# Performance work log

Measured on AMD Instinct MI355X. Metric: run time of the kernel, lower is better.

The kernel has to match this reference:

```python
import jax, jax.numpy as jnp
import numpy as np

CLIP = 100000.0
T, N, C, H, E = 8, 1024, 64, 256, 32768
NC = N * (N + 1) // 2


def _ntn(t):
    return jnp.nan_to_num(t, nan=0.0, posinf=CLIP, neginf=-CLIP)


def _gcn_conv(x, row, col, ew, W, b, n):
    # PyG GCNConv: sym-normalized aggregation (self-loops already appended)
    h = x @ W  # [n, out]
    deg = jax.ops.segment_sum(ew, col, num_segments=n)
    dinv = jnp.where(deg > 0, jax.lax.rsqrt(jnp.where(deg > 0, deg, 1.0)), 0.0)
    norm = dinv[row] * ew * dinv[col]  # [e]
    out = jax.ops.segment_sum(norm[:, None] * h[row], col, num_segments=n)
    return out + b


def setup_inputs() -> dict:
    key = jax.random.key(0)
    ks = jax.random.split(key, 10)
    return {
        "xs": jax.random.normal(ks[0], (T, N, C), jnp.float32),
        "edge_index": jax.random.randint(ks[1], (T, 2, E), 0, N),
        "edge_weight": jax.random.uniform(ks[2], (T, E), jnp.float32),
        "conv1_w": jax.random.normal(ks[3], (C, H), jnp.float32) * 0.05,
        "conv1_b": jnp.zeros((H,), jnp.float32),
        "conv2_w": jax.random.normal(ks[4], (H, H), jnp.float32) * 0.05,
        "conv2_b": jnp.zeros((H,), jnp.float32),
        "w_ih": jax.random.normal(ks[5], (4 * H, H), jnp.float32) * 0.05,
        "w_hh": jax.random.normal(ks[6], (4 * H, H), jnp.float32) * 0.05,
        "b_ih": jnp.zeros((4 * H,), jnp.float32),
        "b_hh": jnp.zeros((4 * H,), jnp.float32),
        "fc_w": jax.random.normal(ks[7], (H, NC), jnp.float32) * 0.02,
        "fc_b": jnp.zeros((NC,), jnp.float32),
    }


def reference(xs, edge_index, edge_weight, conv1_w, conv1_b, conv2_w, conv2_b,
              w_ih, w_hh, b_ih, b_hh, fc_w, fc_b):
    n = xs.shape[1]
    self_idx = jnp.arange(n)

    def per_step(x, ei, ew):
        # add self-loops with weight 1 (GCNConv default)
        row = jnp.concatenate([ei[0], self_idx])
        col = jnp.concatenate([ei[1], self_idx])
        w = jnp.concatenate([ew, jnp.ones((n,), ew.dtype)])
        h = jax.nn.relu(_ntn(_gcn_conv(x, row, col, w, conv1_w, conv1_b, n)))
        h = jax.nn.relu(_ntn(_gcn_conv(h, row, col, w, conv2_w, conv2_b, n)))
        return _ntn(h.mean(axis=0))  # global mean pool, single graph

    embs = _ntn(jax.vmap(per_step)(xs, edge_index, edge_weight))  # [T, H]

    def lstm_step(carry, x_t):
        h, c = carry
        g = x_t @ w_ih.T + b_ih + h @ w_hh.T + b_hh
        i, f, gg, o = jnp.split(g, 4)
        c = jax.nn.sigmoid(f) * c + jax.nn.sigmoid(i) * jnp.tanh(gg)
        h = jax.nn.sigmoid(o) * jnp.tanh(c)
        return (h, c), h

    hdim = w_hh.shape[1]
    init = (jnp.zeros((hdim,), embs.dtype), jnp.zeros((hdim,), embs.dtype))
    _, hs = jax.lax.scan(lstm_step, init, embs)
    final_h = _ntn(_ntn(hs)[-1])  # [H]

    vec = _ntn(final_h @ fc_w + fc_b)  # [N(N+1)/2]
    tril = jnp.tril_indices(n)  # row-major (i, j<=i) matches torch loop
    L = jnp.zeros((n, n), vec.dtype).at[tril].set(vec)
    return _ntn(L @ L.T)
```

## Files before the change

### kernel.cpp

```cpp
#include <hip/hip_runtime.h>
#include <hip/hip_bf16.h>
#include <math.h>

#define T_ 8
#define N_ 1024
#define C_ 64
#define H_ 256
#define E_ 32768
#define NC_ 524800
#define CLIPV 100000.0f

__device__ __forceinline__ float sigmoidf_(float x) { return 1.0f / (1.0f + __expf(-x)); }

__global__ void init_kernel(float* deg, int* cnt, float* cbuf, float* pool_part) {
    int g = blockIdx.x * 256 + threadIdx.x;
    if (g < T_ * N_) { deg[g] = 1.0f; cnt[g] = 0; }
    if (g < 512) cbuf[g] = 0.0f;
    if (g < T_ * 32 * H_) pool_part[g] = 0.0f;
}

__global__ void deg_count_kernel(const int* ei, const float* ew, float* deg, int* cnt) {
    int g = blockIdx.x * 256 + threadIdx.x;
    int t = g >> 15, e = g & (E_ - 1);
    int col = ei[t * 2 * E_ + E_ + e];
    atomicAdd(&deg[t * N_ + col], ew[g]);
    atomicAdd(&cnt[t * N_ + col], 1);
}

__global__ void dinv_kernel(float* deg) {
    int g = blockIdx.x * 256 + threadIdx.x;
    deg[g] = rsqrtf(deg[g]);
}

__global__ __launch_bounds__(1024) void scan_kernel(const int* cnt, int* ptr, int* cursor) {
    __shared__ int s[1024];
    int t = blockIdx.x, tid = threadIdx.x;
    int c0 = cnt[t * N_ + tid];
    s[tid] = c0;
    __syncthreads();
    for (int off = 1; off < 1024; off <<= 1) {
        int v = (tid >= off) ? s[tid - off] : 0;
        __syncthreads();
        s[tid] += v;
        __syncthreads();
    }
    int excl = s[tid] - c0;
    ptr[t * N_ + tid] = excl;
    cursor[t * N_ + tid] = excl;
}

__global__ void scatter_kernel(const int* ei, const float* ew, const float* dinv,
                               int* cursor, int* csr_src, float* csr_nrm) {
    int g = blockIdx.x * 256 + threadIdx.x;
    int t = g >> 15, e = g & (E_ - 1);
    int row = ei[t * 2 * E_ + e];
    int col = ei[t * 2 * E_ + E_ + e];
    int pos = atomicAdd(&cursor[t * N_ + col], 1);
    csr_src[t * E_ + pos] = row;
    csr_nrm[t * E_ + pos] = ew[g] * dinv[t * N_ + row];
}

__global__ __launch_bounds__(256) void sgemm_nn(const float* __restrict__ A,
                                                const float* __restrict__ B,
                                                float* __restrict__ C,
                                                int M, int N, int K) {
    __shared__ float As[16][68];
    __shared__ float Bs[16][68];
    int tid = threadIdx.x;
    int tx = tid & 15, ty = tid >> 4;
    int m0 = blockIdx.y * 64, n0 = blockIdx.x * 64;
    float acc[4][4] = {{0.f}};
    for (int k0 = 0; k0 < K; k0 += 16) {
        int ka = tid & 15, ma = tid >> 4;
#pragma unroll
        for (int mm = 0; mm < 64; mm += 16)
            As[ka][ma + mm] = A[(size_t)(m0 + ma + mm) * K + k0 + ka];
        int nb = tid & 63, kb = tid >> 6;
#pragma unroll
        for (int kk = 0; kk < 16; kk += 4)
            Bs[kb + kk][nb] = B[(size_t)(k0 + kb + kk) * N + n0 + nb];
        __syncthreads();
#pragma unroll
        for (int kk = 0; kk < 16; ++kk) {
            float4 a4 = *(const float4*)&As[kk][ty * 4];
            float4 b4 = *(const float4*)&Bs[kk][tx * 4];
            float a[4] = {a4.x, a4.y, a4.z, a4.w};
            float b[4] = {b4.x, b4.y, b4.z, b4.w};
#pragma unroll
            for (int i = 0; i < 4; ++i)
#pragma unroll
                for (int j = 0; j < 4; ++j) acc[i][j] += a[i] * b[j];
        }
        __syncthreads();
    }
#pragma unroll
    for (int i = 0; i < 4; ++i) {
        float4 o = make_float4(acc[i][0], acc[i][1], acc[i][2], acc[i][3]);
        *(float4*)&C[(size_t)(m0 + ty * 4 + i) * N + n0 + tx * 4] = o;
    }
}

template <bool POOL>
__global__ __launch_bounds__(256) void agg_kernel(const float* __restrict__ hin,
                                                  const float* __restrict__ dinv,
                                                  const int* __restrict__ ptr,
                                                  const int* __restrict__ cnt,
                                                  const int* __restrict__ csr_src,
                                                  const float* __restrict__ csr_nrm,
                                                  const float* __restrict__ bias,
                                                  float* __restrict__ out) {
    __shared__ int s_src[256];
    __shared__ float s_nrm[256];
    int bx = blockIdx.x;
    int t = bx >> 10, j = bx & 1023;
    int c = threadIdx.x;
    float dj = dinv[bx];
    int start = ptr[bx], count = cnt[bx];
    const float* hbase = hin + (size_t)(t * N_) * H_;
    float self = hin[(size_t)bx * H_ + c];
    float accE = 0.0f;
    for (int base = 0; base < count; base += 256) {
        int m = min(256, count - base);
        __syncthreads();
        if (c < m) {
            s_src[c] = csr_src[t * E_ + start + base + c];
            s_nrm[c] = csr_nrm[t * E_ + start + base + c];
        }
        __syncthreads();
        for (int u = 0; u < m; ++u)
            accE += s_nrm[u] * hbase[(size_t)s_src[u] * H_ + c];
    }
    float val = dj * (dj * self + accE) + bias[c];
    val = fminf(fmaxf(val, 0.0f), CLIPV);
    if (POOL)
        atomicAdd(&out[(size_t)(t * 32 + (j & 31)) * H_ + c], val * (1.0f / 1024.0f));
    else
        out[(size_t)bx * H_ + c] = val;
}

__global__ void pool_final_kernel(const float* pool_part, float* embs) {
    int t = blockIdx.x, c = threadIdx.x;
    float a = 0.f;
#pragma unroll
    for (int g2 = 0; g2 < 32; ++g2) a += pool_part[(size_t)(t * 32 + g2) * H_ + c];
    a = fminf(fmaxf(a, -CLIPV), CLIPV);
    embs[t * H_ + c] = a;
}

__global__ __launch_bounds__(256) void xg_kernel(const float* __restrict__ embs,
                                                 const float* __restrict__ w_ih,
                                                 const float* __restrict__ b_ih,
                                                 const float* __restrict__ b_hh,
                                                 float* __restrict__ xg) {
    __shared__ float s_e[H_];
    int b = blockIdx.x;
    int t = b >> 2;
    int j = (b & 3) * 256 + threadIdx.x;
    s_e[threadIdx.x] = embs[t * H_ + threadIdx.x];
    __syncthreads();
    const float4* wr = (const float4*)(w_ih + (size_t)j * H_);
    float acc = b_ih[j] + b_hh[j];
#pragma unroll 4
    for (int k4 = 0; k4 < H_ / 4; ++k4) {
        float4 w = wr[k4];
        acc += w.x * s_e[k4 * 4] + w.y * s_e[k4 * 4 + 1] + w.z * s_e[k4 * 4 + 2] + w.w * s_e[k4 * 4 + 3];
    }
    xg[t * 1024 + j] = acc;
}

__global__ __launch_bounds__(256) void lstm_step_kernel(const float* __restrict__ xg,
                                                        const float* __restrict__ w_hh,
                                                        float* __restrict__ gates,
                                                        float* __restrict__ cbuf,
                                                        float* __restrict__ final_h,
                                                        int step) {
    __shared__ float s_h[H_];
    int tid = threadIdx.x;
    if (step == 0) {
        s_h[tid] = 0.0f;
    } else {
        const float* gp = gates + ((step - 1) & 1) * 1024;
        float gi = gp[tid], gf = gp[256 + tid], gg = gp[512 + tid], go = gp[768 + tid];
        float cprev = cbuf[(step & 1) * 256 + tid];
        float cc = sigmoidf_(gf) * cprev + sigmoidf_(gi) * tanhf(gg);
        float hh = sigmoidf_(go) * tanhf(cc);
        if (blockIdx.x == 0) cbuf[((step + 1) & 1) * 256 + tid] = cc;
        if (step == T_) {
            if (blockIdx.x == 0) final_h[tid] = hh;
            return;
        }
        s_h[tid] = hh;
    }
    __syncthreads();
    int j = blockIdx.x * 256 + tid;
    const float4* wr = (const float4*)(w_hh + (size_t)j * H_);
    float acc = xg[step * 1024 + j];
#pragma unroll 4
    for (int k4 = 0; k4 < H_ / 4; ++k4) {
        float4 w = wr[k4];
        acc += w.x * s_h[k4 * 4] + w.y * s_h[k4 * 4 + 1] + w.z * s_h[k4 * 4 + 2] + w.w * s_h[k4 * 4 + 3];
    }
    gates[(step & 1) * 1024 + j] = acc;
}

__global__ __launch_bounds__(256) void fc_kernel(const float* __restrict__ final_h,
                                                 const float* __restrict__ fc_w,
                                                 const float* __restrict__ fc_b,
                                                 float* __restrict__ vec) {
    __shared__ float s_h[H_];
    s_h[threadIdx.x] = final_h[threadIdx.x];
    __syncthreads();
    int j4 = blockIdx.x * 256 + threadIdx.x;
    if (j4 >= NC_ / 4) return;
    const float4* w4 = (const float4*)fc_w;
    float4 acc = ((const float4*)fc_b)[j4];
#pragma unroll 4
    for (int k = 0; k < H_; ++k) {
        float4 w = w4[(size_t)k * (NC_ / 4) + j4];
        float hk = s_h[k];
        acc.x += hk * w.x; acc.y += hk * w.y; acc.z += hk * w.z; acc.w += hk * w.w;
    }
    acc.x = fminf(fmaxf(acc.x, -CLIPV), CLIPV);
    acc.y = fminf(fmaxf(acc.y, -CLIPV), CLIPV);
    acc.z = fminf(fmaxf(acc.z, -CLIPV), CLIPV);
    acc.w = fminf(fmaxf(acc.w, -CLIPV), CLIPV);
    ((float4*)vec)[j4] = acc;
}

__global__ void build_L_kernel(const float* __restrict__ vec, float* __restrict__ L) {
    int g = blockIdx.x * 256 + threadIdx.x;
    int i = g >> 10, j = g & 1023;
    float v = 0.0f;
    if (j <= i) v = vec[(i * (i + 1)) / 2 + j];
    L[g] = v;
}

__global__ __launch_bounds__(256) void syrk_kernel(const float* __restrict__ L, float* __restrict__ Cout) {
    int b = blockIdx.x;
    int I = (int)((sqrtf(8.0f * b + 1.0f) - 1.0f) * 0.5f);
    while ((I + 1) * (I + 2) / 2 <= b) ++I;
    while (I * (I + 1) / 2 > b) --I;
    int J = b - I * (I + 1) / 2;
    int Klim = (J + 1) * 64;
    int kbeg = blockIdx.y * 256;
    int kend = min(Klim, kbeg + 256);
    if (kbeg >= kend) return;

    __shared__ float As[16][68];
    __shared__ float Bs[16][68];
    int tid = threadIdx.x;
    int tx = tid & 15, ty = tid >> 4;
    int m0 = I * 64, n0 = J * 64;
    float acc[4][4] = {{0.f}};
    for (int k0 = kbeg; k0 < kend; k0 += 16) {
        int ka = tid & 15, ma = tid >> 4;
#pragma unroll
        for (int mm = 0; mm < 64; mm += 16) {
            As[ka][ma + mm] = L[(size_t)(m0 + ma + mm) * 1024 + k0 + ka];
            Bs[ka][ma + mm] = L[(size_t)(n0 + ma + mm) * 1024 + k0 + ka];
        }
        __syncthreads();
#pragma unroll
        for (int kk = 0; kk < 16; ++kk) {
            float4 a4 = *(const float4*)&As[kk][ty * 4];
            float4 b4 = *(const float4*)&Bs[kk][tx * 4];
            float a[4] = {a4.x, a4.y, a4.z, a4.w};
            float bb[4] = {b4.x, b4.y, b4.z, b4.w};
#pragma unroll
            for (int i = 0; i < 4; ++i)
#pragma unroll
                for (int j = 0; j < 4; ++j) acc[i][j] += a[i] * bb[j];
        }
        __syncthreads();
    }
#pragma unroll
    for (int i = 0; i < 4; ++i)
#pragma unroll
        for (int j = 0; j < 4; ++j)
            atomicAdd(&Cout[(size_t)(m0 + ty * 4 + i) * 1024 + n0 + tx * 4 + j], acc[i][j]);
}

__global__ __launch_bounds__(256) void mirror_kernel(float* __restrict__ Cout) {
    int J = blockIdx.x, I = blockIdx.y;
    if (J >= I) return;
    __shared__ float s[64][65];
    int cc = threadIdx.x & 63, r0 = threadIdx.x >> 6;
    for (int r = r0; r < 64; r += 4)
        s[r][cc] = Cout[(size_t)(I * 64 + r) * 1024 + J * 64 + cc];
    __syncthreads();
    for (int r = r0; r < 64; r += 4)
        Cout[(size_t)(J * 64 + r) * 1024 + I * 64 + cc] = s[cc][r];
}

extern "C" void kernel_launch(void* const* d_in, const int* in_sizes, int n_in,
                              void* d_out, int out_size, void* d_ws, size_t ws_size,
                              hipStream_t stream) {
    const float* xs      = (const float*)d_in[0];
    const int*   ei      = (const int*)d_in[1];
    const float* ew      = (const float*)d_in[2];
    const float* conv1_w = (const float*)d_in[3];
    const float* conv1_b = (const float*)d_in[4];
    const float* conv2_w = (const float*)d_in[5];
    const float* conv2_b = (const float*)d_in[6];
    const float* w_ih    = (const float*)d_in[7];
    const float* w_hh    = (const float*)d_in[8];
    const float* b_ih    = (const float*)d_in[9];
    const float* b_hh    = (const float*)d_in[10];
    const float* fc_w    = (const float*)d_in[11];
    const float* fc_b    = (const float*)d_in[12];
    float* out = (float*)d_out;

    float* ws = (float*)d_ws;
    size_t off = 0;
    float* xw1  = ws + off; off += (size_t)T_ * N_ * H_;
    float* h1   = ws + off; off += (size_t)T_ * N_ * H_;
    float* vec  = h1;
    float* Lm   = h1 + NC_;
    float* deg  = ws + off; off += T_ * N_;
    float* csr_nrm = ws + off; off += (size_t)T_ * E_;
    float* pool_part = ws + off; off += T_ * 32 * H_;
    float* embs = ws + off; off += T_ * H_;
    float* xg   = ws + off; off += T_ * 4 * H_;
    float* gates = ws + off; off += 2 * 1024;
    float* cbuf  = ws + off; off += 2 * 256;
    float* final_h = ws + off; off += 256;
    int* cnt    = (int*)(ws + off); off += T_ * N_;
    int* ptr    = (int*)(ws + off); off += T_ * N_;
    int* cursor = (int*)(ws + off); off += T_ * N_;
    int* csr_src = (int*)(ws + off); off += (size_t)T_ * E_;
    (void)ws_size; (void)in_sizes; (void)n_in; (void)out_size;

    init_kernel<<<256, 256, 0, stream>>>(deg, cnt, cbuf, pool_part);
    deg_count_kernel<<<(T_ * E_) / 256, 256, 0, stream>>>(ei, ew, deg, cnt);
    dinv_kernel<<<(T_ * N_) / 256, 256, 0, stream>>>(deg);
    scan_kernel<<<T_, 1024, 0, stream>>>(cnt, ptr, cursor);
    scatter_kernel<<<(T_ * E_) / 256, 256, 0, stream>>>(ei, ew, deg, cursor, csr_src, csr_nrm);

    sgemm_nn<<<dim3(H_ / 64, (T_ * N_) / 64), 256, 0, stream>>>(xs, conv1_w, xw1, T_ * N_, H_, C_);
    agg_kernel<false><<<T_ * N_, 256, 0, stream>>>(xw1, deg, ptr, cnt, csr_src, csr_nrm, conv1_b, h1);
    sgemm_nn<<<dim3(H_ / 64, (T_ * N_) / 64), 256, 0, stream>>>(h1, conv2_w, xw1, T_ * N_, H_, H_);
    agg_kernel<true><<<T_ * N_, 256, 0, stream>>>(xw1, deg, ptr, cnt, csr_src, csr_nrm, conv2_b, pool_part);
    pool_final_kernel<<<T_, 256, 0, stream>>>(pool_part, embs);

    xg_kernel<<<32, 256, 0, stream>>>(embs, w_ih, b_ih, b_hh, xg);
    for (int s = 0; s < T_; ++s)
        lstm_step_kernel<<<4, 256, 0, stream>>>(xg, w_hh, gates, cbuf, final_h, s);
    lstm_step_kernel<<<1, 256, 0, stream>>>(xg, w_hh, gates, cbuf, final_h, T_);

    fc_kernel<<<(NC_ / 4 + 255) / 256, 256, 0, stream>>>(final_h, fc_w, fc_b, vec);
    build_L_kernel<<<(N_ * N_) / 256, 256, 0, stream>>>(vec, Lm);

    hipMemsetAsync(d_out, 0, (size_t)N_ * N_ * sizeof(float), stream);
    syrk_kernel<<<dim3(136, 4), 256, 0, stream>>>(Lm, out);
    mirror_kernel<<<dim3(16, 16), 256, 0, stream>>>(out);
}
```

Measured before the change: 346.5 us.

## Fuse small kernels, persist LSTM with grid barrier, scatter FC directly into L

Several small kernels are merged to cut launch overhead: init becomes a memset, dinv folds into a warp-shuffle scan, pool reduction folds into the xg kernel, and the eight LSTM step launches become one persistent kernel. That kernel keeps w_hh in registers and synchronises its four blocks with a spin-wait global barrier. The FC kernel computes two quads per thread and writes directly into the lower-triangular L matrix, removing the separate build_L pass. The aggregation loop is unrolled by four with independent accumulators, which changes the summation order. The spin barrier assumes all four blocks are co-resident and has a timeout escape.

```diff
diff --git a/kernel.cpp b/kernel.cpp
--- a/kernel.cpp
+++ b/kernel.cpp
@@ -12,13 +12,6 @@
 
 __device__ __forceinline__ float sigmoidf_(float x) { return 1.0f / (1.0f + __expf(-x)); }
 
-__global__ void init_kernel(float* deg, int* cnt, float* cbuf, float* pool_part) {
-    int g = blockIdx.x * 256 + threadIdx.x;
-    if (g < T_ * N_) { deg[g] = 1.0f; cnt[g] = 0; }
-    if (g < 512) cbuf[g] = 0.0f;
-    if (g < T_ * 32 * H_) pool_part[g] = 0.0f;
-}
-
 __global__ void deg_count_kernel(const int* ei, const float* ew, float* deg, int* cnt) {
     int g = blockIdx.x * 256 + threadIdx.x;
     int t = g >> 15, e = g & (E_ - 1);
@@ -27,26 +20,35 @@
     atomicAdd(&cnt[t * N_ + col], 1);
 }
 
-__global__ void dinv_kernel(float* deg) {
-    int g = blockIdx.x * 256 + threadIdx.x;
-    deg[g] = rsqrtf(deg[g]);
-}
-
-__global__ __launch_bounds__(1024) void scan_kernel(const int* cnt, int* ptr, int* cursor) {
-    __shared__ int s[1024];
+__global__ __launch_bounds__(1024) void scan_dinv_kernel(const int* cnt, int* ptr, int* cursor,
+                                                         float* deg) {
+    __shared__ int s_wsum[16];
     int t = blockIdx.x, tid = threadIdx.x;
+    int lane = tid & 63, w = tid >> 6;
     int c0 = cnt[t * N_ + tid];
-    s[tid] = c0;
-    __syncthreads();
-    for (int off = 1; off < 1024; off <<= 1) {
-        int v = (tid >= off) ? s[tid - off] : 0;
-        __syncthreads();
-        s[tid] += v;
-        __syncthreads();
-    }
-    int excl = s[tid] - c0;
+    int x = c0;
+#pragma unroll
+    for (int off = 1; off < 64; off <<= 1) {
+        int v = __shfl_up(x, off);
+        if (lane >= off) x += v;
+    }
+    if (lane == 63) s_wsum[w] = x;
+    __syncthreads();
+    if (tid < 16) {
+        int v = s_wsum[tid];
+#pragma unroll
+        for (int off = 1; off < 16; off <<= 1) {
+            int u = __shfl_up(v, off);
+            if (tid >= off) v += u;
+        }
+        s_wsum[tid] = v;
+    }
+    __syncthreads();
+    int base = (w > 0) ? s_wsum[w - 1] : 0;
+    int excl = base + x - c0;
     ptr[t * N_ + tid] = excl;
     cursor[t * N_ + tid] = excl;
+    deg[t * N_ + tid] = rsqrtf(deg[t * N_ + tid] + 1.0f);
 }
 
 __global__ void scatter_kernel(const int* ei, const float* ew, const float* dinv,
@@ -118,7 +120,7 @@
     int start = ptr[bx], count = cnt[bx];
     const float* hbase = hin + (size_t)(t * N_) * H_;
     float self = hin[(size_t)bx * H_ + c];
-    float accE = 0.0f;
+    float a0 = 0.f, a1 = 0.f, a2 = 0.f, a3 = 0.f;
     for (int base = 0; base < count; base += 256) {
         int m = min(256, count - base);
         __syncthreads();
@@ -127,9 +129,18 @@
             s_nrm[c] = csr_nrm[t * E_ + start + base + c];
         }
         __syncthreads();
-        for (int u = 0; u < m; ++u)
-            accE += s_nrm[u] * hbase[(size_t)s_src[u] * H_ + c];
-    }
+        int u = 0;
+        for (; u + 3 < m; u += 4) {
+            int s0 = s_src[u], s1 = s_src[u + 1], s2 = s_src[u + 2], s3 = s_src[u + 3];
+            float n0 = s_nrm[u], n1 = s_nrm[u + 1], n2 = s_nrm[u + 2], n3 = s_nrm[u + 3];
+            a0 += n0 * hbase[(size_t)s0 * H_ + c];
+            a1 += n1 * hbase[(size_t)s1 * H_ + c];
+            a2 += n2 * hbase[(size_t)s2 * H_ + c];
+            a3 += n3 * hbase[(size_t)s3 * H_ + c];
+        }
+        for (; u < m; ++u) a0 += s_nrm[u] * hbase[(size_t)s_src[u] * H_ + c];
+    }
+    float accE = (a0 + a1) + (a2 + a3);
     float val = dj * (dj * self + accE) + bias[c];
     val = fminf(fmaxf(val, 0.0f), CLIPV);
     if (POOL)
@@ -138,25 +149,20 @@
         out[(size_t)bx * H_ + c] = val;
 }
 
-__global__ void pool_final_kernel(const float* pool_part, float* embs) {
-    int t = blockIdx.x, c = threadIdx.x;
-    float a = 0.f;
-#pragma unroll
-    for (int g2 = 0; g2 < 32; ++g2) a += pool_part[(size_t)(t * 32 + g2) * H_ + c];
-    a = fminf(fmaxf(a, -CLIPV), CLIPV);
-    embs[t * H_ + c] = a;
-}
-
-__global__ __launch_bounds__(256) void xg_kernel(const float* __restrict__ embs,
-                                                 const float* __restrict__ w_ih,
-                                                 const float* __restrict__ b_ih,
-                                                 const float* __restrict__ b_hh,
-                                                 float* __restrict__ xg) {
+__global__ __launch_bounds__(256) void xg_pool_kernel(const float* __restrict__ pool_part,
+                                                      const float* __restrict__ w_ih,
+                                                      const float* __restrict__ b_ih,
+                                                      const float* __restrict__ b_hh,
+                                                      float* __restrict__ xg) {
     __shared__ float s_e[H_];
     int b = blockIdx.x;
     int t = b >> 2;
-    int j = (b & 3) * 256 + threadIdx.x;
-    s_e[threadIdx.x] = embs[t * H_ + threadIdx.x];
+    int tid = threadIdx.x;
+    int j = (b & 3) * 256 + tid;
+    float a = 0.f;
+#pragma unroll
+    for (int g2 = 0; g2 < 32; ++g2) a += pool_part[(size_t)(t * 32 + g2) * H_ + tid];
+    s_e[tid] = fminf(fmaxf(a, -CLIPV), CLIPV);
     __syncthreads();
     const float4* wr = (const float4*)(w_ih + (size_t)j * H_);
     float acc = b_ih[j] + b_hh[j];
@@ -168,71 +174,120 @@
     xg[t * 1024 + j] = acc;
 }
 
-__global__ __launch_bounds__(256) void lstm_step_kernel(const float* __restrict__ xg,
+__device__ __forceinline__ void gbar(int* bar, int target) {
+    __syncthreads();
+    if (threadIdx.x == 0) {
+        __threadfence();
+        __hip_atomic_fetch_add(bar, 1, __ATOMIC_ACQ_REL, __HIP_MEMORY_SCOPE_AGENT);
+        long spin = 0;
+        while (__hip_atomic_load(bar, __ATOMIC_ACQUIRE, __HIP_MEMORY_SCOPE_AGENT) < target) {
+            if (++spin > (1L << 27)) break;
+        }
+    }
+    __syncthreads();
+}
+
+__global__ __launch_bounds__(1024) void lstm_all_kernel(const float* __restrict__ xg,
                                                         const float* __restrict__ w_hh,
-                                                        float* __restrict__ gates,
-                                                        float* __restrict__ cbuf,
-                                                        float* __restrict__ final_h,
-                                                        int step) {
+                                                        float* __restrict__ gbuf,
+                                                        int* __restrict__ bar,
+                                                        float* __restrict__ final_h) {
     __shared__ float s_h[H_];
     int tid = threadIdx.x;
-    if (step == 0) {
-        s_h[tid] = 0.0f;
+    int jl = tid >> 2, q = tid & 3;
+    int j = blockIdx.x * 256 + jl;
+    float4 wreg[16];
+    const float4* wr = (const float4*)(w_hh + (size_t)j * H_ + q * 64);
+#pragma unroll
+    for (int r = 0; r < 16; ++r) wreg[r] = wr[r];
+    float c_reg = 0.f;
+    for (int s = 0; s < T_; ++s) {
+        if (s == 0) {
+            if (tid < 256) s_h[tid] = 0.f;
+        } else {
+            if (tid < 256) {
+                const float* gp = gbuf + ((s - 1) & 1) * 1024;
+                float gi = gp[tid], gf = gp[256 + tid], gg = gp[512 + tid], go = gp[768 + tid];
+                c_reg = sigmoidf_(gf) * c_reg + sigmoidf_(gi) * tanhf(gg);
+                s_h[tid] = sigmoidf_(go) * tanhf(c_reg);
+            }
+        }
+        __syncthreads();
+        float acc = 0.f;
+#pragma unroll
+        for (int r = 0; r < 16; ++r) {
+            float4 w = wreg[r];
+            int k = q * 64 + r * 4;
+            acc += w.x * s_h[k] + w.y * s_h[k + 1] + w.z * s_h[k + 2] + w.w * s_h[k + 3];
+        }
+        acc += __shfl_xor(acc, 1);
+        acc += __shfl_xor(acc, 2);
+        if (q == 0) gbuf[(s & 1) * 1024 + j] = xg[s * 1024 + j] + acc;
+        gbar(bar, 4 * (s + 1));
+    }
+    if (blockIdx.x == 0 && tid < 256) {
+        const float* gp = gbuf + ((T_ - 1) & 1) * 1024;
+        float gi = gp[tid], gf = gp[256 + tid], gg = gp[512 + tid], go = gp[768 + tid];
+        float cc = sigmoidf_(gf) * c_reg + sigmoidf_(gi) * tanhf(gg);
+        final_h[tid] = sigmoidf_(go) * tanhf(cc);
+    }
+}
+
+__device__ __forceinline__ void store_quad(float4 v, int j0, float* __restrict__ Lm) {
+    int i = (int)((sqrtf(8.0f * (float)j0 + 1.0f) - 1.0f) * 0.5f);
+    while ((i + 1) * (i + 2) / 2 <= j0) ++i;
+    while (i * (i + 1) / 2 > j0) --i;
+    int rb = i * (i + 1) / 2, col = j0 - rb;
+    if (col + 3 <= i) {
+        *(float4*)&Lm[(size_t)i * 1024 + col] = v;
     } else {
-        const float* gp = gates + ((step - 1) & 1) * 1024;
-        float gi = gp[tid], gf = gp[256 + tid], gg = gp[512 + tid], go = gp[768 + tid];
-        float cprev = cbuf[(step & 1) * 256 + tid];
-        float cc = sigmoidf_(gf) * cprev + sigmoidf_(gi) * tanhf(gg);
-        float hh = sigmoidf_(go) * tanhf(cc);
-        if (blockIdx.x == 0) cbuf[((step + 1) & 1) * 256 + tid] = cc;
-        if (step == T_) {
-            if (blockIdx.x == 0) final_h[tid] = hh;
-            return;
-        }
-        s_h[tid] = hh;
-    }
-    __syncthreads();
-    int j = blockIdx.x * 256 + tid;
-    const float4* wr = (const float4*)(w_hh + (size_t)j * H_);
-    float acc = xg[step * 1024 + j];
-#pragma unroll 4
-    for (int k4 = 0; k4 < H_ / 4; ++k4) {
-        float4 w = wr[k4];
-        acc += w.x * s_h[k4 * 4] + w.y * s_h[k4 * 4 + 1] + w.z * s_h[k4 * 4 + 2] + w.w * s_h[k4 * 4 + 3];
-    }
-    gates[(step & 1) * 1024 + j] = acc;
+        float vv[4] = {v.x, v.y, v.z, v.w};
+#pragma unroll
+        for (int e = 0; e < 4; ++e) {
+            int jj = j0 + e;
+            while ((i + 1) * (i + 2) / 2 <= jj) ++i;
+            Lm[(size_t)i * 1024 + (jj - i * (i + 1) / 2)] = vv[e];
+        }
+    }
 }
 
 __global__ __launch_bounds__(256) void fc_kernel(const float* __restrict__ final_h,
                                                  const float* __restrict__ fc_w,
                                                  const float* __restrict__ fc_b,
-                                                 float* __restrict__ vec) {
+                                                 float* __restrict__ Lm) {
     __shared__ float s_h[H_];
-    s_h[threadIdx.x] = final_h[threadIdx.x];
-    __syncthreads();
-    int j4 = blockIdx.x * 256 + threadIdx.x;
-    if (j4 >= NC_ / 4) return;
+    int tid = threadIdx.x;
+    s_h[tid] = final_h[tid];
+    __syncthreads();
+    const int NQ = NC_ / 4;
+    int j4a = blockIdx.x * 512 + tid;
+    int j4b = j4a + 256;
+    bool va = j4a < NQ, vb = j4b < NQ;
+    int j4b_eff = vb ? j4b : j4a;
+    if (!va) return;
     const float4* w4 = (const float4*)fc_w;
-    float4 acc = ((const float4*)fc_b)[j4];
+    float4 accA = ((const float4*)fc_b)[j4a];
+    float4 accB = vb ? ((const float4*)fc_b)[j4b] : accA;
 #pragma unroll 4
     for (int k = 0; k < H_; ++k) {
-        float4 w = w4[(size_t)k * (NC_ / 4) + j4];
         float hk = s_h[k];
-        acc.x += hk * w.x; acc.y += hk * w.y; acc.z += hk * w.z; acc.w += hk * w.w;
-    }
-    acc.x = fminf(fmaxf(acc.x, -CLIPV), CLIPV);
-    acc.y = fminf(fmaxf(acc.y, -CLIPV), CLIPV);
-    acc.z = fminf(fmaxf(acc.z, -CLIPV), CLIPV);
-    acc.w = fminf(fmaxf(acc.w, -CLIPV), CLIPV);
-    ((float4*)vec)[j4] = acc;
-}
-
-__global__ void build_L_kernel(const float* __restrict__ vec, float* __restrict__ L) {
-    int g = blockIdx.x * 256 + threadIdx.x;
-    int i = g >> 10, j = g & 1023;
-    float v = 0.0f;
-    if (j <= i) v = vec[(i * (i + 1)) / 2 + j];
-    L[g] = v;
+        float4 wa = w4[(size_t)k * NQ + j4a];
+        float4 wb = w4[(size_t)k * NQ + j4b_eff];
+        accA.x += hk * wa.x; accA.y += hk * wa.y; accA.z += hk * wa.z; accA.w += hk * wa.w;
+        accB.x += hk * wb.x; accB.y += hk * wb.y; accB.z += hk * wb.z; accB.w += hk * wb.w;
+    }
+    accA.x = fminf(fmaxf(accA.x, -CLIPV), CLIPV);
+    accA.y = fminf(fmaxf(accA.y, -CLIPV), CLIPV);
+    accA.z = fminf(fmaxf(accA.z, -CLIPV), CLIPV);
+    accA.w = fminf(fmaxf(accA.w, -CLIPV), CLIPV);
+    store_quad(accA, j4a * 4, Lm);
+    if (vb) {
+        accB.x = fminf(fmaxf(accB.x, -CLIPV), CLIPV);
+        accB.y = fminf(fmaxf(accB.y, -CLIPV), CLIPV);
+        accB.z = fminf(fmaxf(accB.z, -CLIPV), CLIPV);
+        accB.w = fminf(fmaxf(accB.w, -CLIPV), CLIPV);
+        store_quad(accB, j4b * 4, Lm);
+    }
 }
 
 __global__ __launch_bounds__(256) void syrk_kernel(const float* __restrict__ L, float* __restrict__ Cout) {
@@ -314,41 +369,37 @@
     size_t off = 0;
     float* xw1  = ws + off; off += (size_t)T_ * N_ * H_;
     float* h1   = ws + off; off += (size_t)T_ * N_ * H_;
-    float* vec  = h1;
-    float* Lm   = h1 + NC_;
+    float* Lm   = h1;
     float* deg  = ws + off; off += T_ * N_;
+    int*   cnt  = (int*)(ws + off); off += T_ * N_;
+    float* pool_part = ws + off; off += T_ * 32 * H_;
+    int*   bar  = (int*)(ws + off); off += 256;
+    size_t zero_bytes = ((size_t)(T_ * N_) * 2 + T_ * 32 * H_ + 256) * 4;
+    float* zero_base = deg;
     float* csr_nrm = ws + off; off += (size_t)T_ * E_;
-    float* pool_part = ws + off; off += T_ * 32 * H_;
-    float* embs = ws + off; off += T_ * H_;
     float* xg   = ws + off; off += T_ * 4 * H_;
-    float* gates = ws + off; off += 2 * 1024;
-    float* cbuf  = ws + off; off += 2 * 256;
+    float* gbuf = ws + off; off += 2 * 1024;
     float* final_h = ws + off; off += 256;
-    int* cnt    = (int*)(ws + off); off += T_ * N_;
     int* ptr    = (int*)(ws + off); off += T_ * N_;
     int* cursor = (int*)(ws + off); off += T_ * N_;
     int* csr_src = (int*)(ws + off); off += (size_t)T_ * E_;
     (void)ws_size; (void)in_sizes; (void)n_in; (void)out_size;
 
-    init_kernel<<<256, 256, 0, stream>>>(deg, cnt, cbuf, pool_part);
+    hipMemsetAsync(zero_base, 0, zero_bytes, stream);
     deg_count_kernel<<<(T_ * E_) / 256, 256, 0, stream>>>(ei, ew, deg, cnt);
-    dinv_kernel<<<(T_ * N_) / 256, 256, 0, stream>>>(deg);
-    scan_kernel<<<T_, 1024, 0, stream>>>(cnt, ptr, cursor);
+    scan_dinv_kernel<<<T_, 1024, 0, stream>>>(cnt, ptr, cursor, deg);
     scatter_kernel<<<(T_ * E_) / 256, 256, 0, stream>>>(ei, ew, deg, cursor, csr_src, csr_nrm);
 
     sgemm_nn<<<dim3(H_ / 64, (T_ * N_) / 64), 256, 0, stream>>>(xs, conv1_w, xw1, T_ * N_, H_, C_);
     agg_kernel<false><<<T_ * N_, 256, 0, stream>>>(xw1, deg, ptr, cnt, csr_src, csr_nrm, conv1_b, h1);
     sgemm_nn<<<dim3(H_ / 64, (T_ * N_) / 64), 256, 0, stream>>>(h1, conv2_w, xw1, T_ * N_, H_, H_);
     agg_kernel<true><<<T_ * N_, 256, 0, stream>>>(xw1, deg, ptr, cnt, csr_src, csr_nrm, conv2_b, pool_part);
-    pool_final_kernel<<<T_, 256, 0, stream>>>(pool_part, embs);
-
-    xg_kernel<<<32, 256, 0, stream>>>(embs, w_ih, b_ih, b_hh, xg);
-    for (int s = 0; s < T_; ++s)
-        lstm_step_kernel<<<4, 256, 0, stream>>>(xg, w_hh, gates, cbuf, final_h, s);
-    lstm_step_kernel<<<1, 256, 0, stream>>>(xg, w_hh, gates, cbuf, final_h, T_);
-
-    fc_kernel<<<(NC_ / 4 + 255) / 256, 256, 0, stream>>>(final_h, fc_w, fc_b, vec);
-    build_L_kernel<<<(N_ * N_) / 256, 256, 0, stream>>>(vec, Lm);
+
+    xg_pool_kernel<<<32, 256, 0, stream>>>(pool_part, w_ih, b_ih, b_hh, xg);
+    lstm_all_kernel<<<4, 1024, 0, stream>>>(xg, w_hh, gbuf, bar, final_h);
+
+    hipMemsetAsync(Lm, 0, (size_t)N_ * N_ * sizeof(float), stream);
+    fc_kernel<<<(NC_ / 4 + 511) / 512, 256, 0, stream>>>(final_h, fc_w, fc_b, Lm);
 
     hipMemsetAsync(d_out, 0, (size_t)N_ * N_ * sizeof(float), stream);
     syrk_kernel<<<dim3(136, 4), 256, 0, stream>>>(Lm, out);
```

New measurement: 322.0 us. 1.08x faster.
